# Kernel tuning notes

Measured on AMD Instinct MI355X. Metric: run time of the kernel, lower is better.

Reference implementation:

```python
import jax, jax.numpy as jnp
import numpy as np
import math

N = 30000; N0 = 18000; N1 = 12000; R = 5; E = 600000
H = 128; HM = 128; C = 8
L1 = 20.0; L2 = 30.0
THRESH = 0.3; THRESH_C = 1e-3
T_INNER = 20; K_OUTER = 8
EPS = 1e-5


def setup_inputs() -> dict:
    key = jax.random.key(0)
    ks = jax.random.split(key, 16)
    def w(k, shape):  # kaiming-ish fan_in init
        return jax.random.normal(k, shape, jnp.float32) / np.sqrt(shape[0])
    return {
        "feat0": jax.random.normal(ks[0], (N0, 256), jnp.float32),
        "feat1": jax.random.normal(ks[1], (N1, 128), jnp.float32),
        "W0": w(ks[2], (256, H)), "b0": jnp.zeros((H,), jnp.float32),
        "W1": w(ks[3], (128, H)), "b1": jnp.zeros((H,), jnp.float32),
        "Wm1": w(ks[4], (H, HM)), "bm1": jnp.zeros((HM,), jnp.float32),
        "Wm2": w(ks[5], (HM, HM)), "bm2": jnp.zeros((HM,), jnp.float32),
        "Wout": w(ks[6], (HM, C)), "bout": jnp.zeros((C,), jnp.float32),
        "src": jax.random.randint(ks[7], (E,), 0, N, jnp.int32),
        "dst": jax.random.randint(ks[8], (E,), 0, N, jnp.int32),
        "rel": jax.random.randint(ks[9], (E,), 0, R, jnp.int32),
    }


def _layernorm(z):
    m = z.mean(-1, keepdims=True)
    v = z.var(-1, keepdims=True)
    return (z - m) / jnp.sqrt(v + EPS)


def _forward(feat0, feat1, W0, b0, W1, b1, Wm1, bm1, Wm2, bm2, Wout, bout, src, dst, rel):
    # transfer (transf_type==2): per-type linear -> concat -> 2-layer MLP w/ layernorm
    h = jnp.concatenate([feat0 @ W0 + b0, feat1 @ W1 + b1], axis=0)   # (N, H)
    z = jax.nn.relu(_layernorm(h @ Wm1 + bm1))
    h = z @ Wm2 + bm2                                                 # (N, HM)
    # per-node standardization (torch std is unbiased, ddof=1), nan -> 0
    mu = h.mean(1, keepdims=True)
    sd = h.std(1, ddof=1, keepdims=True)
    out0 = jnp.nan_to_num((h - mu) / sd)

    # per-relation row degrees of the vertically stacked adjacency (R*N, N)
    key_e = rel * N + src                                             # (E,)
    deg = jax.ops.segment_sum(jnp.ones(E, jnp.float32), key_e, num_segments=R * N)
    safe = jnp.maximum(deg, 1.0)
    vals = jnp.where(deg > 0, 1.0 / safe, 0.0)[key_e]                 # row-normalized A weights
    dinv = jnp.where(deg > 0, 1.0 / jnp.sqrt(safe), 0.0)              # D^{-1/2}
    edge_dinv = dinv[key_e] * dinv[rel * N + dst]                     # (E,)
    active = (deg > 0).astype(jnp.float32).reshape(R, N)              # (R, N)

    def tv(x):  # relational total variation tr(X^T L_r X)/N, L_r = I - D^-1/2 A_r D^-1/2
        node_term = active @ (x * x).sum(1)                           # (R,)
        edot = (x[src] * x[dst]).sum(1)                               # (E,)
        edge_term = jax.ops.segment_sum(edge_dinv * edot, rel, num_segments=R)
        return (node_term - edge_term) / N

    ratio = 2.0 * L2 / L1
    c_l1tr = jnp.abs(tv(out0)).sum()
    u0 = jnp.full((R,), 1.0 / R, jnp.float32)

    def mirror_descent(u, w, l1tr):
        fi = l1tr + ratio
        def step(carry, t):
            u, act = carry
            T_t = jnp.sqrt(2.0 * math.log(R) / (t * fi * fi))
            u_ta = u * jnp.exp(-T_t * (ratio * u + w))
            u_new = u_ta / u_ta.sum()
            diff = jnp.sqrt(((u - u_new) ** 2).sum())
            u = jnp.where(act, u_new, u)
            return (u, act & (diff >= THRESH_C)), None
        ts = jnp.arange(1, T_INNER + 1, dtype=jnp.float32)
        (u, _), _ = jax.lax.scan(step, (u, jnp.array(True)), ts)
        return u

    def outer(carry, _):
        x, u, act = carry
        w = tv(x)
        l1tr = jnp.abs(w).sum()
        u = jnp.where(act, mirror_descent(u, w, l1tr), u)
        still = act & (l1tr / c_l1tr >= THRESH)
        ew = u[rel] * vals                                            # (E,)
        msg = jax.ops.segment_sum(ew[:, None] * x[dst], src, num_segments=N)  # (N, HM)
        x = jnp.where(still, x / (1.0 + L1) + (L1 / (1.0 + L1)) * msg, x)
        return (x, u, still), None

    (x, u, _), _ = jax.lax.scan(outer, (out0, u0, jnp.array(True)), None, length=K_OUTER)
    logits = x @ Wout + bout
    return logits, x, u


def reference(feat0, feat1, W0, b0, W1, b1, Wm1, bm1, Wm2, bm2, Wout, bout, src, dst, rel):
    return _forward(feat0, feat1, W0, b0, W1, b1, Wm1, bm1, Wm2, bm2, Wout, bout, src, dst, rel)
```

## Files before the change

### kernel.cpp

```cpp
#include <hip/hip_runtime.h>
#include <hip/hip_fp16.h>
#include <cmath>

typedef unsigned short ushort_t;
typedef unsigned int uint_t;

#define N_TOT 30000
#define N0_   18000
#define R_    5
#define E_    600000
#define RN    (R_ * N_TOT)
#define NC_   (N_TOT * 8)
#define NX_   (N_TOT * 128)
#define NL_   (N_TOT * 64)
#define SCAN_NB ((RN + 1023) / 1024)

typedef __attribute__((ext_vector_type(8))) short bf16x8;
typedef __attribute__((ext_vector_type(4))) float f32x4;

__device__ __forceinline__ ushort_t f2bf(float f) {
    uint_t u = __float_as_uint(f);
    uint_t r = (u + 0x7fffu + ((u >> 16) & 1u)) >> 16;
    return (ushort_t)r;
}
__device__ __forceinline__ float bflo(uint_t v) { return __uint_as_float(v << 16); }
__device__ __forceinline__ float bfhi(uint_t v) { return __uint_as_float(v & 0xffff0000u); }

__global__ void init_kernel(float* ug, int* act) {
    if (threadIdx.x < 5) ug[threadIdx.x] = 0.2f;
    if (threadIdx.x == 0) act[0] = 1;
}

__global__ __launch_bounds__(256) void cvtfeat_kernel(const float* __restrict__ in,
                                                      ushort_t* __restrict__ out,
                                                      int nelem)
{
    int i = (blockIdx.x * 256 + threadIdx.x) * 4;
    if (i >= nelem) return;
    const float4 v = *(const float4*)(in + i);
    ushort_t o0 = f2bf(v.x), o1 = f2bf(v.y), o2 = f2bf(v.z), o3 = f2bf(v.w);
    uint_t p0 = (uint_t)o0 | ((uint_t)o1 << 16);
    uint_t p1 = (uint_t)o2 | ((uint_t)o3 << 16);
    uint2* op = (uint2*)(out + i);
    *op = make_uint2(p0, p1);
}

__global__ __launch_bounds__(256) void cvtw_kernel(const float* __restrict__ W,
                                                   ushort_t* __restrict__ wt, int K)
{
    int idx = blockIdx.x * 256 + threadIdx.x;
    if (idx >= 128 * K) return;
    int j = idx / K, k = idx - j * K;
    wt[idx] = f2bf(W[k * 128 + j]);
}

__global__ __launch_bounds__(256) void mlp_mfma_kernel(
    const ushort_t* __restrict__ fb0, const ushort_t* __restrict__ fb1,
    const ushort_t* __restrict__ wt0, const ushort_t* __restrict__ wt1,
    const ushort_t* __restrict__ wtm1, const ushort_t* __restrict__ wtm2,
    const float* __restrict__ b0, const float* __restrict__ b1,
    const float* __restrict__ bm1, const float* __restrict__ bm2,
    float* __restrict__ xout, ushort_t* __restrict__ xh)
{
    const int t = threadIdx.x;
    const int lane = t & 63;
    const int wv = t >> 6;
    const int lr = lane & 15;
    const int lg = lane >> 4;
    const int row0 = blockIdx.x * 32;

    __shared__ ushort_t hls[32][136];
    __shared__ float    tls[32][132];
    __shared__ ushort_t zls[32][136];

    #pragma unroll
    for (int mt = 0; mt < 2; ++mt) {
        const int rb = row0 + mt * 16;
        const bool is0 = (rb < N0_);
        const int r = min(rb + lr, N_TOT - 1);
        const ushort_t* __restrict__ fa =
            is0 ? fb0 + (size_t)r * 256 : fb1 + (size_t)(r - N0_) * 128;
        const ushort_t* __restrict__ wt = is0 ? wt0 : wt1;
        const int K = is0 ? 256 : 128;
        const int c0 = wv * 32 + lr;

        f32x4 a0 = {0.f, 0.f, 0.f, 0.f};
        f32x4 a1 = {0.f, 0.f, 0.f, 0.f};
        for (int ks = 0; ks < K; ks += 32) {
            const bf16x8 af = *(const bf16x8*)(fa + ks + lg * 8);
            const bf16x8 wb0 = *(const bf16x8*)(wt + (size_t)c0 * K + ks + lg * 8);
            const bf16x8 wb1 = *(const bf16x8*)(wt + (size_t)(c0 + 16) * K + ks + lg * 8);
            a0 = __builtin_amdgcn_mfma_f32_16x16x32_bf16(af, wb0, a0, 0, 0, 0);
            a1 = __builtin_amdgcn_mfma_f32_16x16x32_bf16(af, wb1, a1, 0, 0, 0);
        }
        const float bb0 = is0 ? b0[c0] : b1[c0];
        const float bb1 = is0 ? b0[c0 + 16] : b1[c0 + 16];
        #pragma unroll
        for (int j = 0; j < 4; ++j) {
            hls[mt * 16 + lg * 4 + j][c0]      = f2bf(a0[j] + bb0);
            hls[mt * 16 + lg * 4 + j][c0 + 16] = f2bf(a1[j] + bb1);
        }
    }
    __syncthreads();

    {
        const int c0 = wv * 32 + lr;
        f32x4 g00 = {0.f,0.f,0.f,0.f}, g01 = {0.f,0.f,0.f,0.f};
        f32x4 g10 = {0.f,0.f,0.f,0.f}, g11 = {0.f,0.f,0.f,0.f};
        for (int ks = 0; ks < 128; ks += 32) {
            const bf16x8 wb0 = *(const bf16x8*)(wtm1 + (size_t)c0 * 128 + ks + lg * 8);
            const bf16x8 wb1 = *(const bf16x8*)(wtm1 + (size_t)(c0 + 16) * 128 + ks + lg * 8);
            const bf16x8 af0 = *(const bf16x8*)(&hls[lr][ks + lg * 8]);
            const bf16x8 af1 = *(const bf16x8*)(&hls[16 + lr][ks + lg * 8]);
            g00 = __builtin_amdgcn_mfma_f32_16x16x32_bf16(af0, wb0, g00, 0, 0, 0);
            g01 = __builtin_amdgcn_mfma_f32_16x16x32_bf16(af0, wb1, g01, 0, 0, 0);
            g10 = __builtin_amdgcn_mfma_f32_16x16x32_bf16(af1, wb0, g10, 0, 0, 0);
            g11 = __builtin_amdgcn_mfma_f32_16x16x32_bf16(af1, wb1, g11, 0, 0, 0);
        }
        const float bb0 = bm1[c0], bb1 = bm1[c0 + 16];
        #pragma unroll
        for (int j = 0; j < 4; ++j) {
            tls[lg * 4 + j][c0]           = g00[j] + bb0;
            tls[lg * 4 + j][c0 + 16]      = g01[j] + bb1;
            tls[16 + lg * 4 + j][c0]      = g10[j] + bb0;
            tls[16 + lg * 4 + j][c0 + 16] = g11[j] + bb1;
        }
    }
    __syncthreads();

    {
        const int row = t >> 3, seg = t & 7;
        f32x4 v[4];
        float s = 0.f;
        #pragma unroll
        for (int i = 0; i < 4; ++i) {
            v[i] = *(const f32x4*)(&tls[row][seg * 16 + i * 4]);
            s += v[i][0] + v[i][1] + v[i][2] + v[i][3];
        }
        #pragma unroll
        for (int o = 1; o < 8; o <<= 1) s += __shfl_xor(s, o, 64);
        const float mean = s * (1.0f / 128.0f);
        float q = 0.f;
        #pragma unroll
        for (int i = 0; i < 4; ++i) {
            #pragma unroll
            for (int e = 0; e < 4; ++e) { float d = v[i][e] - mean; q = fmaf(d, d, q); }
        }
        #pragma unroll
        for (int o = 1; o < 8; o <<= 1) q += __shfl_xor(q, o, 64);
        const float inv = 1.0f / sqrtf(q * (1.0f / 128.0f) + 1e-5f);
        uint_t* zp = (uint_t*)&zls[row][0];
        #pragma unroll
        for (int i = 0; i < 4; ++i) {
            ushort_t z0 = f2bf(fmaxf((v[i][0] - mean) * inv, 0.0f));
            ushort_t z1 = f2bf(fmaxf((v[i][1] - mean) * inv, 0.0f));
            ushort_t z2 = f2bf(fmaxf((v[i][2] - mean) * inv, 0.0f));
            ushort_t z3 = f2bf(fmaxf((v[i][3] - mean) * inv, 0.0f));
            zp[(seg * 16 + i * 4) / 2]     = (uint_t)z0 | ((uint_t)z1 << 16);
            zp[(seg * 16 + i * 4) / 2 + 1] = (uint_t)z2 | ((uint_t)z3 << 16);
        }
    }
    __syncthreads();

    {
        const int c0 = wv * 32 + lr;
        f32x4 g00 = {0.f,0.f,0.f,0.f}, g01 = {0.f,0.f,0.f,0.f};
        f32x4 g10 = {0.f,0.f,0.f,0.f}, g11 = {0.f,0.f,0.f,0.f};
        for (int ks = 0; ks < 128; ks += 32) {
            const bf16x8 wb0 = *(const bf16x8*)(wtm2 + (size_t)c0 * 128 + ks + lg * 8);
            const bf16x8 wb1 = *(const bf16x8*)(wtm2 + (size_t)(c0 + 16) * 128 + ks + lg * 8);
            const bf16x8 af0 = *(const bf16x8*)(&zls[lr][ks + lg * 8]);
            const bf16x8 af1 = *(const bf16x8*)(&zls[16 + lr][ks + lg * 8]);
            g00 = __builtin_amdgcn_mfma_f32_16x16x32_bf16(af0, wb0, g00, 0, 0, 0);
            g01 = __builtin_amdgcn_mfma_f32_16x16x32_bf16(af0, wb1, g01, 0, 0, 0);
            g10 = __builtin_amdgcn_mfma_f32_16x16x32_bf16(af1, wb0, g10, 0, 0, 0);
            g11 = __builtin_amdgcn_mfma_f32_16x16x32_bf16(af1, wb1, g11, 0, 0, 0);
        }
        __syncthreads();
        const float bb0 = bm2[c0], bb1 = bm2[c0 + 16];
        #pragma unroll
        for (int j = 0; j < 4; ++j) {
            tls[lg * 4 + j][c0]           = g00[j] + bb0;
            tls[lg * 4 + j][c0 + 16]      = g01[j] + bb1;
            tls[16 + lg * 4 + j][c0]      = g10[j] + bb0;
            tls[16 + lg * 4 + j][c0 + 16] = g11[j] + bb1;
        }
    }
    __syncthreads();

    {
        const int row = t >> 3, seg = t & 7;
        const int n = row0 + row;
        f32x4 v[4];
        float s = 0.f;
        #pragma unroll
        for (int i = 0; i < 4; ++i) {
            v[i] = *(const f32x4*)(&tls[row][seg * 16 + i * 4]);
            s += v[i][0] + v[i][1] + v[i][2] + v[i][3];
        }
        #pragma unroll
        for (int o = 1; o < 8; o <<= 1) s += __shfl_xor(s, o, 64);
        const float mu = s * (1.0f / 128.0f);
        float q = 0.f;
        #pragma unroll
        for (int i = 0; i < 4; ++i) {
            #pragma unroll
            for (int e = 0; e < 4; ++e) { float d = v[i][e] - mu; q = fmaf(d, d, q); }
        }
        #pragma unroll
        for (int o = 1; o < 8; o <<= 1) q += __shfl_xor(q, o, 64);
        const float sd = sqrtf(q * (1.0f / 127.0f));
        const float inv = 1.0f / sd;
        if (n < N_TOT) {
            uint_t* xhp = (uint_t*)xh + (size_t)n * 64 + seg * 8;
            float* xop = xout + (size_t)n * 128 + seg * 16;
            #pragma unroll
            for (int i = 0; i < 4; ++i) {
                float rr[4];
                #pragma unroll
                for (int e = 0; e < 4; ++e) {
                    float r = (v[i][e] - mu) * inv;
                    if (!(fabsf(r) <= 3.402823466e38f)) {
                        r = (r != r) ? 0.0f : ((r > 0.0f) ? 3.402823466e38f : -3.402823466e38f);
                    }
                    rr[e] = r;
                }
                *(float4*)(xop + i * 4) = make_float4(rr[0], rr[1], rr[2], rr[3]);
                xhp[i * 2]     = (uint_t)f2bf(rr[0]) | ((uint_t)f2bf(rr[1]) << 16);
                xhp[i * 2 + 1] = (uint_t)f2bf(rr[2]) | ((uint_t)f2bf(rr[3]) << 16);
            }
        }
    }
}

__global__ void deg_kernel(const int* __restrict__ src, const int* __restrict__ rel,
                           int* __restrict__ deg_i)
{
    int e = blockIdx.x * 256 + threadIdx.x;
    if (e >= E_) return;
    atomicAdd(&deg_i[src[e] * R_ + rel[e]], 1);
}

__global__ void dinv_kernel(const int* __restrict__ deg_i, float* __restrict__ dinv)
{
    int i = blockIdx.x * 256 + threadIdx.x;
    if (i >= RN) return;
    int dg = deg_i[i];
    dinv[i] = (dg > 0) ? 1.0f / sqrtf((float)dg) : 0.0f;
}

__global__ __launch_bounds__(256) void scan1_kernel(const int* __restrict__ cnt,
                                                    int* __restrict__ rp,
                                                    int* __restrict__ bsum)
{
    __shared__ int wsum[4];
    const int t = threadIdx.x, lane = t & 63, w = t >> 6;
    const int i0 = blockIdx.x * 1024 + t * 4;
    const int v0 = (i0 + 0 < RN) ? cnt[i0 + 0] : 0;
    const int v1 = (i0 + 1 < RN) ? cnt[i0 + 1] : 0;
    const int v2 = (i0 + 2 < RN) ? cnt[i0 + 2] : 0;
    const int v3 = (i0 + 3 < RN) ? cnt[i0 + 3] : 0;
    const int s = v0 + v1 + v2 + v3;
    int sc = s;
    #pragma unroll
    for (int o = 1; o < 64; o <<= 1) { int tmp = __shfl_up(sc, o, 64); if (lane >= o) sc += tmp; }
    if (lane == 63) wsum[w] = sc;
    __syncthreads();
    int woff = 0;
    #pragma unroll
    for (int i = 0; i < 3; ++i) if (i < w) woff += wsum[i];
    int run = woff + sc - s;
    if (i0 + 0 < RN) rp[i0 + 0] = run; run += v0;
    if (i0 + 1 < RN) rp[i0 + 1] = run; run += v1;
    if (i0 + 2 < RN) rp[i0 + 2] = run; run += v2;
    if (i0 + 3 < RN) rp[i0 + 3] = run;
    if (t == 255) bsum[blockIdx.x] = woff + sc;
}

__global__ __launch_bounds__(256) void scan2_kernel(const int* __restrict__ bsum,
                                                    int* __restrict__ boff,
                                                    int* __restrict__ rp)
{
    __shared__ int wsum[4];
    const int t = threadIdx.x, lane = t & 63, w = t >> 6;
    const int v = (t < SCAN_NB) ? bsum[t] : 0;
    int sc = v;
    #pragma unroll
    for (int o = 1; o < 64; o <<= 1) { int tmp = __shfl_up(sc, o, 64); if (lane >= o) sc += tmp; }
    if (lane == 63) wsum[w] = sc;
    __syncthreads();
    int woff = 0;
    #pragma unroll
    for (int i = 0; i < 3; ++i) if (i < w) woff += wsum[i];
    boff[t] = woff + sc - v;
    if (t == 0) rp[RN] = E_;
}

__global__ __launch_bounds__(256) void scan3_kernel(int* __restrict__ rp,
                                                    const int* __restrict__ boff)
{
    const int off = boff[blockIdx.x];
    if (off == 0) return;
    const int i0 = blockIdx.x * 1024 + threadIdx.x * 4;
    if (i0 + 3 < RN) {
        int4* p = (int4*)(rp + i0);
        int4 q = *p;
        q.x += off; q.y += off; q.z += off; q.w += off;
        *p = q;
    } else {
        for (int i = 0; i < 4; ++i)
            if (i0 + i < RN) rp[i0 + i] += off;
    }
}

__global__ void scatter_kernel(const int* __restrict__ src, const int* __restrict__ dst,
                               const int* __restrict__ rel, const int* __restrict__ rp,
                               int* __restrict__ fill, const int* __restrict__ deg_i,
                               const float* __restrict__ dinv,
                               int4* __restrict__ csr_pk)
{
    int e = blockIdx.x * 256 + threadIdx.x;
    if (e >= E_) return;
    int s = src[e], r = rel[e], d = dst[e];
    int key = s * R_ + r;
    int pos = rp[key] + atomicAdd(&fill[key], 1);
    float edinv = dinv[key] * dinv[d * R_ + r];
    float w = 1.0f / (float)deg_i[key];
    csr_pk[pos] = make_int4(d, __float_as_int(edinv), __float_as_int(w), 0);
}

__global__ __launch_bounds__(256) void gather_kernel(
    const ushort_t* __restrict__ xh, const int* __restrict__ rp,
    const int4* __restrict__ csr_pk,
    const int* __restrict__ act, int k, float* __restrict__ accbuf,
    uint_t* __restrict__ mbuf)
{
    if (act[k] == 0) return;
    const int lane = threadIdx.x & 63;
    const int wv = threadIdx.x >> 6;
    const int wid = blockIdx.x * 4 + wv;
    const int nw = gridDim.x * 4;
    float na[5] = {0, 0, 0, 0, 0};
    float ea[5] = {0, 0, 0, 0, 0};
    for (int n = wid; n < N_TOT; n += nw) {
        const int b0 = __builtin_amdgcn_readfirstlane(rp[n * R_ + 0]);
        const int b1 = __builtin_amdgcn_readfirstlane(rp[n * R_ + 1]);
        const int b2 = __builtin_amdgcn_readfirstlane(rp[n * R_ + 2]);
        const int b3 = __builtin_amdgcn_readfirstlane(rp[n * R_ + 3]);
        const int b4 = __builtin_amdgcn_readfirstlane(rp[n * R_ + 4]);
        const int b5 = __builtin_amdgcn_readfirstlane(rp[n * R_ + 5]);
        const uint_t vs = ((const uint_t*)(xh + (size_t)n * 128))[lane];
        const float sx = bflo(vs), sy = bfhi(vs);
        const float pp = fmaf(sx, sx, sy * sy);
        if (b1 > b0) na[0] += pp;
        if (b2 > b1) na[1] += pp;
        if (b3 > b2) na[2] += pp;
        if (b4 > b3) na[3] += pp;
        if (b5 > b4) na[4] += pp;
        float mx[5] = {0, 0, 0, 0, 0};
        float my[5] = {0, 0, 0, 0, 0};
        int e = b0;
        for (; e + 4 <= b5; e += 4) {
            int4 p0 = csr_pk[e + 0];
            int4 p1 = csr_pk[e + 1];
            int4 p2 = csr_pk[e + 2];
            int4 p3 = csr_pk[e + 3];
            const uint_t v0 = ((const uint_t*)(xh + (size_t)p0.x * 128))[lane];
            const uint_t v1 = ((const uint_t*)(xh + (size_t)p1.x * 128))[lane];
            const uint_t v2 = ((const uint_t*)(xh + (size_t)p2.x * 128))[lane];
            const uint_t v3 = ((const uint_t*)(xh + (size_t)p3.x * 128))[lane];
            const float x0 = bflo(v0), y0 = bfhi(v0);
            const float x1 = bflo(v1), y1 = bfhi(v1);
            const float x2 = bflo(v2), y2 = bfhi(v2);
            const float x3 = bflo(v3), y3 = bfhi(v3);
            const float d0 = __int_as_float(p0.y) * fmaf(sx, x0, sy * y0);
            const float d1 = __int_as_float(p1.y) * fmaf(sx, x1, sy * y1);
            const float d2 = __int_as_float(p2.y) * fmaf(sx, x2, sy * y2);
            const float d3 = __int_as_float(p3.y) * fmaf(sx, x3, sy * y3);
            const int r0 = (e + 0 >= b1) + (e + 0 >= b2) + (e + 0 >= b3) + (e + 0 >= b4);
            const int r1 = (e + 1 >= b1) + (e + 1 >= b2) + (e + 1 >= b3) + (e + 1 >= b4);
            const int r2 = (e + 2 >= b1) + (e + 2 >= b2) + (e + 2 >= b3) + (e + 2 >= b4);
            const int r3 = (e + 3 >= b1) + (e + 3 >= b2) + (e + 3 >= b3) + (e + 3 >= b4);
            #pragma unroll
            for (int rr = 0; rr < 5; ++rr) {
                ea[rr] += (r0 == rr ? d0 : 0.0f) + (r1 == rr ? d1 : 0.0f) +
                          (r2 == rr ? d2 : 0.0f) + (r3 == rr ? d3 : 0.0f);
                const float ws0 = (r0 == rr) ? __int_as_float(p0.z) : 0.0f;
                const float ws1 = (r1 == rr) ? __int_as_float(p1.z) : 0.0f;
                const float ws2 = (r2 == rr) ? __int_as_float(p2.z) : 0.0f;
                const float ws3 = (r3 == rr) ? __int_as_float(p3.z) : 0.0f;
                mx[rr] = fmaf(ws0, x0, fmaf(ws1, x1, fmaf(ws2, x2, fmaf(ws3, x3, mx[rr]))));
                my[rr] = fmaf(ws0, y0, fmaf(ws1, y1, fmaf(ws2, y2, fmaf(ws3, y3, my[rr]))));
            }
        }
        for (; e < b5; ++e) {
            int4 p0 = csr_pk[e];
            const uint_t v0 = ((const uint_t*)(xh + (size_t)p0.x * 128))[lane];
            const float x0 = bflo(v0), y0 = bfhi(v0);
            const float d0 = __int_as_float(p0.y) * fmaf(sx, x0, sy * y0);
            const int r0 = (e >= b1) + (e >= b2) + (e >= b3) + (e >= b4);
            #pragma unroll
            for (int rr = 0; rr < 5; ++rr) {
                ea[rr] += (r0 == rr ? d0 : 0.0f);
                const float ws0 = (r0 == rr) ? __int_as_float(p0.z) : 0.0f;
                mx[rr] = fmaf(ws0, x0, mx[rr]);
                my[rr] = fmaf(ws0, y0, my[rr]);
            }
        }
        #pragma unroll
        for (int rr = 0; rr < 5; ++rr) {
            __half2 hm = __floats2half2_rn(mx[rr], my[rr]);
            mbuf[(size_t)rr * NL_ + (size_t)n * 64 + lane] =
                *reinterpret_cast<const uint_t*>(&hm);
        }
    }
    __shared__ float sacc[4][10];
    #pragma unroll
    for (int r = 0; r < 5; ++r) {
        float a = na[r], b = ea[r];
        for (int o = 32; o > 0; o >>= 1) {
            a += __shfl_down(a, o, 64);
            b += __shfl_down(b, o, 64);
        }
        if (lane == 0) { sacc[wv][r] = a; sacc[wv][5 + r] = b; }
    }
    __syncthreads();
    if (threadIdx.x < 10) {
        float t = sacc[0][threadIdx.x] + sacc[1][threadIdx.x] +
                  sacc[2][threadIdx.x] + sacc[3][threadIdx.x];
        atomicAdd(&accbuf[k * 16 + threadIdx.x], t);
    }
}

__global__ void scalar_kernel(const float* __restrict__ accbuf, float* __restrict__ ug,
                              float* __restrict__ c_l1, int* __restrict__ act, int k)
{
    if (blockIdx.x != 0 || threadIdx.x >= 8) return;
    const int r = threadIdx.x;
    const int a = act[k];
    float w = (r < 5) ? (accbuf[k * 16 + r] - accbuf[k * 16 + 5 + r]) * (1.0f / 30000.0f)
                      : 0.0f;
    float l1 = fabsf(w);
    for (int o = 4; o > 0; o >>= 1) l1 += __shfl_xor(l1, o, 8);
    if (k == 0 && r == 0) c_l1[0] = l1;
    if (!a) { if (r == 0) act[k + 1] = 0; return; }
    float u = (r < 5) ? ug[r] : 0.0f;
    const float fi = l1 + 3.0f;
    bool mact = true;
    for (int t = 1; t <= 20; ++t) {
        float T = sqrtf(3.2188758248682006f / ((float)t * fi * fi));
        float ta = u * expf(-T * (3.0f * u + w));
        float ssum = ta;
        for (int o = 4; o > 0; o >>= 1) ssum += __shfl_xor(ssum, o, 8);
        float un = ta / ssum;
        float d0 = u - un;
        float dq = d0 * d0;
        for (int o = 4; o > 0; o >>= 1) dq += __shfl_xor(dq, o, 8);
        if (mact) u = un;
        mact = mact && (sqrtf(dq) >= 1e-3f);
    }
    if (r < 5) ug[r] = u;
    if (r == 0) act[k + 1] = (l1 / c_l1[0] >= 0.3f) ? 1 : 0;
}

__global__ __launch_bounds__(256) void apply_kernel(
    float* __restrict__ x, ushort_t* __restrict__ xh_out,
    const uint_t* __restrict__ mbuf, const float* __restrict__ ug,
    const int* __restrict__ act, int k)
{
    if (act[k + 1] == 0) return;
    const int tid = blockIdx.x * 256 + threadIdx.x;
    if (tid >= NL_) return;
    const float u0 = ug[0], u1 = ug[1], u2 = ug[2], u3 = ug[3], u4 = ug[4];

    uint_t w0 = mbuf[(size_t)0 * NL_ + tid];
    uint_t w1 = mbuf[(size_t)1 * NL_ + tid];
    uint_t w2 = mbuf[(size_t)2 * NL_ + tid];
    uint_t w3 = mbuf[(size_t)3 * NL_ + tid];
    uint_t w4 = mbuf[(size_t)4 * NL_ + tid];
    const float2 m0 = __half22float2(*reinterpret_cast<const __half2*>(&w0));
    const float2 m1 = __half22float2(*reinterpret_cast<const __half2*>(&w1));
    const float2 m2 = __half22float2(*reinterpret_cast<const __half2*>(&w2));
    const float2 m3 = __half22float2(*reinterpret_cast<const __half2*>(&w3));
    const float2 m4 = __half22float2(*reinterpret_cast<const __half2*>(&w4));

    const float sm_x = u0 * m0.x + u1 * m1.x + u2 * m2.x + u3 * m3.x + u4 * m4.x;
    const float sm_y = u0 * m0.y + u1 * m1.y + u2 * m2.y + u3 * m3.y + u4 * m4.y;

    const float ci = 1.0f / 21.0f, cb = 20.0f / 21.0f;
    float2* xp = (float2*)x;
    const float2 xs = xp[tid];
    const float nx_ = fmaf(cb, sm_x, xs.x * ci);
    const float ny_ = fmaf(cb, sm_y, xs.y * ci);
    xp[tid] = make_float2(nx_, ny_);
    ((uint_t*)xh_out)[tid] = ((uint_t)f2bf(ny_) << 16) | (uint_t)f2bf(nx_);
}

__global__ __launch_bounds__(256) void final_kernel(const float* __restrict__ x,
                                                    const float* __restrict__ Wout,
                                                    const float* __restrict__ bout,
                                                    const float* __restrict__ ug,
                                                    float* __restrict__ out)
{
    const int nl = threadIdx.x >> 7;
    const int n = blockIdx.x * 2 + nl;
    const int j = threadIdx.x & 127;
    const int lane = threadIdx.x & 63;
    const int wv = threadIdx.x >> 6;
    float xv = x[(size_t)n * 128 + j];
    out[(size_t)NC_ + (size_t)n * 128 + j] = xv;
    float p[8];
    #pragma unroll
    for (int c = 0; c < 8; ++c) p[c] = xv * Wout[j * 8 + c];
    #pragma unroll
    for (int c = 0; c < 8; ++c)
        for (int o = 32; o > 0; o >>= 1) p[c] += __shfl_down(p[c], o, 64);
    __shared__ float sp[4][8];
    if (lane == 0) {
        #pragma unroll
        for (int c = 0; c < 8; ++c) sp[wv][c] = p[c];
    }
    __syncthreads();
    if (j < 8) {
        int c = j;
        out[(size_t)n * 8 + c] = bout[c] + sp[2 * nl][c] + sp[2 * nl + 1][c];
    }
    if (blockIdx.x == 0 && threadIdx.x < 5)
        out[(size_t)NC_ + (size_t)NX_ + threadIdx.x] = ug[threadIdx.x];
}

extern "C" void kernel_launch(void* const* d_in, const int* in_sizes, int n_in,
                              void* d_out, int out_size, void* d_ws, size_t ws_size,
                              hipStream_t stream)
{
    const float* feat0 = (const float*)d_in[0];
    const float* feat1 = (const float*)d_in[1];
    const float* W0   = (const float*)d_in[2];
    const float* b0   = (const float*)d_in[3];
    const float* W1   = (const float*)d_in[4];
    const float* b1   = (const float*)d_in[5];
    const float* Wm1  = (const float*)d_in[6];
    const float* bm1  = (const float*)d_in[7];
    const float* Wm2  = (const float*)d_in[8];
    const float* bm2  = (const float*)d_in[9];
    const float* Wout = (const float*)d_in[10];
    const float* bout = (const float*)d_in[11];
    const int* src = (const int*)d_in[12];
    const int* dst = (const int*)d_in[13];
    const int* rel = (const int*)d_in[14];
    float* out = (float*)d_out;

    char* p = (char*)d_ws;
    auto alloc = [&](size_t bytes) { char* q = p; p += (bytes + 255) & ~(size_t)255; return q; };
    float*    xbuf      = (float*)   alloc((size_t)NX_ * 4);
    ushort_t* xh0       = (ushort_t*)alloc((size_t)NX_ * 2);
    ushort_t* xh1       = (ushort_t*)alloc((size_t)NX_ * 2);
    uint_t*   mbuf      = (uint_t*)  alloc((size_t)R_ * NL_ * 4);
    ushort_t* fb0       = (ushort_t*)alloc((size_t)N0_ * 256 * 2);
    ushort_t* fb1       = (ushort_t*)alloc((size_t)(N_TOT - N0_) * 128 * 2);
    ushort_t* wt0       = (ushort_t*)alloc((size_t)128 * 256 * 2);
    ushort_t* wt1       = (ushort_t*)alloc((size_t)128 * 128 * 2);
    ushort_t* wtm1      = (ushort_t*)alloc((size_t)128 * 128 * 2);
    ushort_t* wtm2      = (ushort_t*)alloc((size_t)128 * 128 * 2);
    int*      deg_i     = (int*)     alloc((size_t)RN * 4);
    float*    dinv      = (float*)   alloc((size_t)RN * 4);
    int*      rp        = (int*)     alloc(((size_t)RN + 1) * 4);
    int*      fill      = (int*)     alloc((size_t)RN * 4);
    int*      bsum      = (int*)     alloc((size_t)SCAN_NB * 4);
    int*      boff      = (int*)     alloc(256 * 4);
    int4*     csr_pk    = (int4*)    alloc((size_t)E_ * 16);
    float*    accbuf    = (float*)   alloc(128 * 4);
    float*    ug        = (float*)   alloc(64);
    float*    c_l1      = (float*)   alloc(64);
    int*      act       = (int*)     alloc(64);

    hipMemsetAsync(deg_i, 0, (size_t)RN * 4, stream);
    hipMemsetAsync(fill, 0, (size_t)RN * 4, stream);
    hipMemsetAsync(accbuf, 0, 128 * 4, stream);
    init_kernel<<<1, 64, 0, stream>>>(ug, act);

    cvtfeat_kernel<<<(N0_ * 256 / 4 + 255) / 256, 256, 0, stream>>>(feat0, fb0, N0_ * 256);
    cvtfeat_kernel<<<((N_TOT - N0_) * 128 / 4 + 255) / 256, 256, 0, stream>>>(
        feat1, fb1, (N_TOT - N0_) * 128);
    cvtw_kernel<<<(128 * 256 + 255) / 256, 256, 0, stream>>>(W0, wt0, 256);
    cvtw_kernel<<<(128 * 128 + 255) / 256, 256, 0, stream>>>(W1, wt1, 128);
    cvtw_kernel<<<(128 * 128 + 255) / 256, 256, 0, stream>>>(Wm1, wtm1, 128);
    cvtw_kernel<<<(128 * 128 + 255) / 256, 256, 0, stream>>>(Wm2, wtm2, 128);

    mlp_mfma_kernel<<<(N_TOT + 31) / 32, 256, 0, stream>>>(
        fb0, fb1, wt0, wt1, wtm1, wtm2, b0, b1, bm1, bm2, xbuf, xh0);

    deg_kernel<<<(E_ + 255) / 256, 256, 0, stream>>>(src, rel, deg_i);
    dinv_kernel<<<(RN + 255) / 256, 256, 0, stream>>>(deg_i, dinv);
    scan1_kernel<<<SCAN_NB, 256, 0, stream>>>(deg_i, rp, bsum);
    scan2_kernel<<<1, 256, 0, stream>>>(bsum, boff, rp);
    scan3_kernel<<<SCAN_NB, 256, 0, stream>>>(rp, boff);
    scatter_kernel<<<(E_ + 255) / 256, 256, 0, stream>>>(src, dst, rel, rp, fill,
                                                         deg_i, dinv, csr_pk);

    ushort_t* ha = xh0;
    ushort_t* hb = xh1;
    for (int k = 0; k < 8; ++k) {
        gather_kernel<<<2048, 256, 0, stream>>>(ha, rp, csr_pk, act, k, accbuf, mbuf);
        scalar_kernel<<<1, 64, 0, stream>>>(accbuf, ug, c_l1, act, k);
        apply_kernel<<<(NL_ + 255) / 256, 256, 0, stream>>>(xbuf, hb, mbuf, ug, act, k);
        ushort_t* t = ha; ha = hb; hb = t;
    }

    final_kernel<<<N_TOT / 2, 256, 0, stream>>>(xbuf, Wout, bout, ug, out);
}
```

Measured before the change: 434.0 us.

## Fuse mirror-descent scalar kernel into apply kernel and add nontemporal loads/stores

Removes the single-block scalar kernel launch per outer iteration. Every thread of the apply kernel now redundantly computes the 5-way mirror-descent update, and the u state is double-buffered so that no block reads a value another block is writing. Nontemporal loads and stores are added for the CSR stream, the message buffer and x, and the gather grid grows from 2048 to 2500 blocks. In exchange, each apply thread runs 20 iterations of five expf calls, which adds redundant ALU work across all threads.

```diff
diff --git a/kernel.cpp b/kernel.cpp
--- a/kernel.cpp
+++ b/kernel.cpp
@@ -17,6 +17,8 @@
 
 typedef __attribute__((ext_vector_type(8))) short bf16x8;
 typedef __attribute__((ext_vector_type(4))) float f32x4;
+typedef __attribute__((ext_vector_type(2))) float f32x2;
+typedef __attribute__((ext_vector_type(4))) int int4v;
 
 __device__ __forceinline__ ushort_t f2bf(float f) {
     uint_t u = __float_as_uint(f);
@@ -26,9 +28,13 @@
 __device__ __forceinline__ float bflo(uint_t v) { return __uint_as_float(v << 16); }
 __device__ __forceinline__ float bfhi(uint_t v) { return __uint_as_float(v & 0xffff0000u); }
 
-__global__ void init_kernel(float* ug, int* act) {
-    if (threadIdx.x < 5) ug[threadIdx.x] = 0.2f;
-    if (threadIdx.x == 0) act[0] = 1;
+__global__ void init_kernel(float* ug, float* ufin, int* act) {
+    if (threadIdx.x < 16) act[threadIdx.x] = (threadIdx.x == 0) ? 1 : 0;
+    if (threadIdx.x < 5) {
+        ug[threadIdx.x] = 0.2f;
+        ug[8 + threadIdx.x] = 0.2f;
+        ufin[threadIdx.x] = 0.2f;
+    }
 }
 
 __global__ __launch_bounds__(256) void cvtfeat_kernel(const float* __restrict__ in,
@@ -331,11 +337,12 @@
 
 __global__ __launch_bounds__(256) void gather_kernel(
     const ushort_t* __restrict__ xh, const int* __restrict__ rp,
-    const int4* __restrict__ csr_pk,
+    const int* __restrict__ csr_pk_raw,
     const int* __restrict__ act, int k, float* __restrict__ accbuf,
     uint_t* __restrict__ mbuf)
 {
     if (act[k] == 0) return;
+    const int4v* __restrict__ csr_pk = (const int4v*)csr_pk_raw;
     const int lane = threadIdx.x & 63;
     const int wv = threadIdx.x >> 6;
     const int wid = blockIdx.x * 4 + wv;
@@ -361,22 +368,22 @@
         float my[5] = {0, 0, 0, 0, 0};
         int e = b0;
         for (; e + 4 <= b5; e += 4) {
-            int4 p0 = csr_pk[e + 0];
-            int4 p1 = csr_pk[e + 1];
-            int4 p2 = csr_pk[e + 2];
-            int4 p3 = csr_pk[e + 3];
-            const uint_t v0 = ((const uint_t*)(xh + (size_t)p0.x * 128))[lane];
-            const uint_t v1 = ((const uint_t*)(xh + (size_t)p1.x * 128))[lane];
-            const uint_t v2 = ((const uint_t*)(xh + (size_t)p2.x * 128))[lane];
-            const uint_t v3 = ((const uint_t*)(xh + (size_t)p3.x * 128))[lane];
+            int4v p0 = __builtin_nontemporal_load(csr_pk + e + 0);
+            int4v p1 = __builtin_nontemporal_load(csr_pk + e + 1);
+            int4v p2 = __builtin_nontemporal_load(csr_pk + e + 2);
+            int4v p3 = __builtin_nontemporal_load(csr_pk + e + 3);
+            const uint_t v0 = ((const uint_t*)(xh + (size_t)p0[0] * 128))[lane];
+            const uint_t v1 = ((const uint_t*)(xh + (size_t)p1[0] * 128))[lane];
+            const uint_t v2 = ((const uint_t*)(xh + (size_t)p2[0] * 128))[lane];
+            const uint_t v3 = ((const uint_t*)(xh + (size_t)p3[0] * 128))[lane];
             const float x0 = bflo(v0), y0 = bfhi(v0);
             const float x1 = bflo(v1), y1 = bfhi(v1);
             const float x2 = bflo(v2), y2 = bfhi(v2);
             const float x3 = bflo(v3), y3 = bfhi(v3);
-            const float d0 = __int_as_float(p0.y) * fmaf(sx, x0, sy * y0);
-            const float d1 = __int_as_float(p1.y) * fmaf(sx, x1, sy * y1);
-            const float d2 = __int_as_float(p2.y) * fmaf(sx, x2, sy * y2);
-            const float d3 = __int_as_float(p3.y) * fmaf(sx, x3, sy * y3);
+            const float d0 = __int_as_float(p0[1]) * fmaf(sx, x0, sy * y0);
+            const float d1 = __int_as_float(p1[1]) * fmaf(sx, x1, sy * y1);
+            const float d2 = __int_as_float(p2[1]) * fmaf(sx, x2, sy * y2);
+            const float d3 = __int_as_float(p3[1]) * fmaf(sx, x3, sy * y3);
             const int r0 = (e + 0 >= b1) + (e + 0 >= b2) + (e + 0 >= b3) + (e + 0 >= b4);
             const int r1 = (e + 1 >= b1) + (e + 1 >= b2) + (e + 1 >= b3) + (e + 1 >= b4);
             const int r2 = (e + 2 >= b1) + (e + 2 >= b2) + (e + 2 >= b3) + (e + 2 >= b4);
@@ -385,24 +392,24 @@
             for (int rr = 0; rr < 5; ++rr) {
                 ea[rr] += (r0 == rr ? d0 : 0.0f) + (r1 == rr ? d1 : 0.0f) +
                           (r2 == rr ? d2 : 0.0f) + (r3 == rr ? d3 : 0.0f);
-                const float ws0 = (r0 == rr) ? __int_as_float(p0.z) : 0.0f;
-                const float ws1 = (r1 == rr) ? __int_as_float(p1.z) : 0.0f;
-                const float ws2 = (r2 == rr) ? __int_as_float(p2.z) : 0.0f;
-                const float ws3 = (r3 == rr) ? __int_as_float(p3.z) : 0.0f;
+                const float ws0 = (r0 == rr) ? __int_as_float(p0[2]) : 0.0f;
+                const float ws1 = (r1 == rr) ? __int_as_float(p1[2]) : 0.0f;
+                const float ws2 = (r2 == rr) ? __int_as_float(p2[2]) : 0.0f;
+                const float ws3 = (r3 == rr) ? __int_as_float(p3[2]) : 0.0f;
                 mx[rr] = fmaf(ws0, x0, fmaf(ws1, x1, fmaf(ws2, x2, fmaf(ws3, x3, mx[rr]))));
                 my[rr] = fmaf(ws0, y0, fmaf(ws1, y1, fmaf(ws2, y2, fmaf(ws3, y3, my[rr]))));
             }
         }
         for (; e < b5; ++e) {
-            int4 p0 = csr_pk[e];
-            const uint_t v0 = ((const uint_t*)(xh + (size_t)p0.x * 128))[lane];
+            int4v p0 = __builtin_nontemporal_load(csr_pk + e);
+            const uint_t v0 = ((const uint_t*)(xh + (size_t)p0[0] * 128))[lane];
             const float x0 = bflo(v0), y0 = bfhi(v0);
-            const float d0 = __int_as_float(p0.y) * fmaf(sx, x0, sy * y0);
+            const float d0 = __int_as_float(p0[1]) * fmaf(sx, x0, sy * y0);
             const int r0 = (e >= b1) + (e >= b2) + (e >= b3) + (e >= b4);
             #pragma unroll
             for (int rr = 0; rr < 5; ++rr) {
                 ea[rr] += (r0 == rr ? d0 : 0.0f);
-                const float ws0 = (r0 == rr) ? __int_as_float(p0.z) : 0.0f;
+                const float ws0 = (r0 == rr) ? __int_as_float(p0[2]) : 0.0f;
                 mx[rr] = fmaf(ws0, x0, mx[rr]);
                 my[rr] = fmaf(ws0, y0, my[rr]);
             }
@@ -410,8 +417,8 @@
         #pragma unroll
         for (int rr = 0; rr < 5; ++rr) {
             __half2 hm = __floats2half2_rn(mx[rr], my[rr]);
-            mbuf[(size_t)rr * NL_ + (size_t)n * 64 + lane] =
-                *reinterpret_cast<const uint_t*>(&hm);
+            __builtin_nontemporal_store(*reinterpret_cast<const uint_t*>(&hm),
+                mbuf + (size_t)rr * NL_ + (size_t)n * 64 + lane);
         }
     }
     __shared__ float sacc[4][10];
@@ -432,74 +439,81 @@
     }
 }
 
-__global__ void scalar_kernel(const float* __restrict__ accbuf, float* __restrict__ ug,
-                              float* __restrict__ c_l1, int* __restrict__ act, int k)
-{
-    if (blockIdx.x != 0 || threadIdx.x >= 8) return;
-    const int r = threadIdx.x;
-    const int a = act[k];
-    float w = (r < 5) ? (accbuf[k * 16 + r] - accbuf[k * 16 + 5 + r]) * (1.0f / 30000.0f)
-                      : 0.0f;
-    float l1 = fabsf(w);
-    for (int o = 4; o > 0; o >>= 1) l1 += __shfl_xor(l1, o, 8);
-    if (k == 0 && r == 0) c_l1[0] = l1;
-    if (!a) { if (r == 0) act[k + 1] = 0; return; }
-    float u = (r < 5) ? ug[r] : 0.0f;
+__global__ __launch_bounds__(256) void apply_kernel(
+    float* __restrict__ x, ushort_t* __restrict__ xh_out,
+    const uint_t* __restrict__ mbuf, const float* __restrict__ accbuf,
+    float* __restrict__ ug, float* __restrict__ ufin, float* __restrict__ c_l1,
+    int* __restrict__ act, int k)
+{
+    if (act[k] == 0) return;
+    float wr[5], l1 = 0.0f;
+    #pragma unroll
+    for (int r = 0; r < 5; ++r) {
+        wr[r] = (accbuf[k * 16 + r] - accbuf[k * 16 + 5 + r]) * (1.0f / 30000.0f);
+        l1 += fabsf(wr[r]);
+    }
+    const float cl1 = (k == 0) ? l1 : c_l1[0];
+    const float* us = ug + (k & 1) * 8;
+    float v0 = us[0], v1 = us[1], v2 = us[2], v3 = us[3], v4 = us[4];
     const float fi = l1 + 3.0f;
     bool mact = true;
     for (int t = 1; t <= 20; ++t) {
-        float T = sqrtf(3.2188758248682006f / ((float)t * fi * fi));
-        float ta = u * expf(-T * (3.0f * u + w));
-        float ssum = ta;
-        for (int o = 4; o > 0; o >>= 1) ssum += __shfl_xor(ssum, o, 8);
-        float un = ta / ssum;
-        float d0 = u - un;
-        float dq = d0 * d0;
-        for (int o = 4; o > 0; o >>= 1) dq += __shfl_xor(dq, o, 8);
-        if (mact) u = un;
+        const float T = sqrtf(3.2188758248682006f / ((float)t * fi * fi));
+        const float t0 = v0 * expf(-T * (3.0f * v0 + wr[0]));
+        const float t1 = v1 * expf(-T * (3.0f * v1 + wr[1]));
+        const float t2 = v2 * expf(-T * (3.0f * v2 + wr[2]));
+        const float t3 = v3 * expf(-T * (3.0f * v3 + wr[3]));
+        const float t4 = v4 * expf(-T * (3.0f * v4 + wr[4]));
+        const float inv = 1.0f / (t0 + t1 + t2 + t3 + t4);
+        const float n0 = t0 * inv, n1 = t1 * inv, n2 = t2 * inv,
+                    n3 = t3 * inv, n4 = t4 * inv;
+        const float dq = (v0 - n0) * (v0 - n0) + (v1 - n1) * (v1 - n1) +
+                         (v2 - n2) * (v2 - n2) + (v3 - n3) * (v3 - n3) +
+                         (v4 - n4) * (v4 - n4);
+        if (mact) { v0 = n0; v1 = n1; v2 = n2; v3 = n3; v4 = n4; }
         mact = mact && (sqrtf(dq) >= 1e-3f);
     }
-    if (r < 5) ug[r] = u;
-    if (r == 0) act[k + 1] = (l1 / c_l1[0] >= 0.3f) ? 1 : 0;
-}
-
-__global__ __launch_bounds__(256) void apply_kernel(
-    float* __restrict__ x, ushort_t* __restrict__ xh_out,
-    const uint_t* __restrict__ mbuf, const float* __restrict__ ug,
-    const int* __restrict__ act, int k)
-{
-    if (act[k + 1] == 0) return;
+    const bool still = (l1 / cl1 >= 0.3f);
+    if (blockIdx.x == 0 && threadIdx.x == 0) {
+        float* ud = ug + ((k + 1) & 1) * 8;
+        ud[0] = v0; ud[1] = v1; ud[2] = v2; ud[3] = v3; ud[4] = v4;
+        ufin[0] = v0; ufin[1] = v1; ufin[2] = v2; ufin[3] = v3; ufin[4] = v4;
+        act[k + 1] = still ? 1 : 0;
+        if (k == 0) c_l1[0] = l1;
+    }
+    if (!still) return;
+
     const int tid = blockIdx.x * 256 + threadIdx.x;
     if (tid >= NL_) return;
-    const float u0 = ug[0], u1 = ug[1], u2 = ug[2], u3 = ug[3], u4 = ug[4];
-
-    uint_t w0 = mbuf[(size_t)0 * NL_ + tid];
-    uint_t w1 = mbuf[(size_t)1 * NL_ + tid];
-    uint_t w2 = mbuf[(size_t)2 * NL_ + tid];
-    uint_t w3 = mbuf[(size_t)3 * NL_ + tid];
-    uint_t w4 = mbuf[(size_t)4 * NL_ + tid];
+
+    uint_t w0 = __builtin_nontemporal_load(mbuf + (size_t)0 * NL_ + tid);
+    uint_t w1 = __builtin_nontemporal_load(mbuf + (size_t)1 * NL_ + tid);
+    uint_t w2 = __builtin_nontemporal_load(mbuf + (size_t)2 * NL_ + tid);
+    uint_t w3 = __builtin_nontemporal_load(mbuf + (size_t)3 * NL_ + tid);
+    uint_t w4 = __builtin_nontemporal_load(mbuf + (size_t)4 * NL_ + tid);
     const float2 m0 = __half22float2(*reinterpret_cast<const __half2*>(&w0));
     const float2 m1 = __half22float2(*reinterpret_cast<const __half2*>(&w1));
     const float2 m2 = __half22float2(*reinterpret_cast<const __half2*>(&w2));
     const float2 m3 = __half22float2(*reinterpret_cast<const __half2*>(&w3));
     const float2 m4 = __half22float2(*reinterpret_cast<const __half2*>(&w4));
 
-    const float sm_x = u0 * m0.x + u1 * m1.x + u2 * m2.x + u3 * m3.x + u4 * m4.x;
-    const float sm_y = u0 * m0.y + u1 * m1.y + u2 * m2.y + u3 * m3.y + u4 * m4.y;
+    const float sm_x = v0 * m0.x + v1 * m1.x + v2 * m2.x + v3 * m3.x + v4 * m4.x;
+    const float sm_y = v0 * m0.y + v1 * m1.y + v2 * m2.y + v3 * m3.y + v4 * m4.y;
 
     const float ci = 1.0f / 21.0f, cb = 20.0f / 21.0f;
-    float2* xp = (float2*)x;
-    const float2 xs = xp[tid];
-    const float nx_ = fmaf(cb, sm_x, xs.x * ci);
-    const float ny_ = fmaf(cb, sm_y, xs.y * ci);
-    xp[tid] = make_float2(nx_, ny_);
+    f32x2* xp = (f32x2*)x;
+    const f32x2 xs = __builtin_nontemporal_load(xp + tid);
+    const float nx_ = fmaf(cb, sm_x, xs[0] * ci);
+    const float ny_ = fmaf(cb, sm_y, xs[1] * ci);
+    f32x2 xn; xn[0] = nx_; xn[1] = ny_;
+    __builtin_nontemporal_store(xn, xp + tid);
     ((uint_t*)xh_out)[tid] = ((uint_t)f2bf(ny_) << 16) | (uint_t)f2bf(nx_);
 }
 
 __global__ __launch_bounds__(256) void final_kernel(const float* __restrict__ x,
                                                     const float* __restrict__ Wout,
                                                     const float* __restrict__ bout,
-                                                    const float* __restrict__ ug,
+                                                    const float* __restrict__ ufin,
                                                     float* __restrict__ out)
 {
     const int nl = threadIdx.x >> 7;
@@ -526,7 +540,7 @@
         out[(size_t)n * 8 + c] = bout[c] + sp[2 * nl][c] + sp[2 * nl + 1][c];
     }
     if (blockIdx.x == 0 && threadIdx.x < 5)
-        out[(size_t)NC_ + (size_t)NX_ + threadIdx.x] = ug[threadIdx.x];
+        out[(size_t)NC_ + (size_t)NX_ + threadIdx.x] = ufin[threadIdx.x];
 }
 
 extern "C" void kernel_launch(void* const* d_in, const int* in_sizes, int n_in,
@@ -571,13 +585,14 @@
     int4*     csr_pk    = (int4*)    alloc((size_t)E_ * 16);
     float*    accbuf    = (float*)   alloc(128 * 4);
     float*    ug        = (float*)   alloc(64);
+    float*    ufin      = (float*)   alloc(64);
     float*    c_l1      = (float*)   alloc(64);
     int*      act       = (int*)     alloc(64);
 
     hipMemsetAsync(deg_i, 0, (size_t)RN * 4, stream);
     hipMemsetAsync(fill, 0, (size_t)RN * 4, stream);
     hipMemsetAsync(accbuf, 0, 128 * 4, stream);
-    init_kernel<<<1, 64, 0, stream>>>(ug, act);
+    init_kernel<<<1, 64, 0, stream>>>(ug, ufin, act);
 
     cvtfeat_kernel<<<(N0_ * 256 / 4 + 255) / 256, 256, 0, stream>>>(feat0, fb0, N0_ * 256);
     cvtfeat_kernel<<<((N_TOT - N0_) * 128 / 4 + 255) / 256, 256, 0, stream>>>(
@@ -601,11 +616,12 @@
     ushort_t* ha = xh0;
     ushort_t* hb = xh1;
     for (int k = 0; k < 8; ++k) {
-        gather_kernel<<<2048, 256, 0, stream>>>(ha, rp, csr_pk, act, k, accbuf, mbuf);
-        scalar_kernel<<<1, 64, 0, stream>>>(accbuf, ug, c_l1, act, k);
-        apply_kernel<<<(NL_ + 255) / 256, 256, 0, stream>>>(xbuf, hb, mbuf, ug, act, k);
+        gather_kernel<<<2500, 256, 0, stream>>>(ha, rp, (const int*)csr_pk,
+                                                act, k, accbuf, mbuf);
+        apply_kernel<<<(NL_ + 255) / 256, 256, 0, stream>>>(
+            xbuf, hb, mbuf, accbuf, ug, ufin, c_l1, act, k);
         ushort_t* t = ha; ha = hb; hb = t;
     }
 
-    final_kernel<<<N_TOT / 2, 256, 0, stream>>>(xbuf, Wout, bout, ug, out);
-}
+    final_kernel<<<N_TOT / 2, 256, 0, stream>>>(xbuf, Wout, bout, ufin, out);
+}
```

Result: slower. 686.3 us (+58.1%).
